# Kernel tuning notes

Hardware: AMD Instinct MI355X
Metric: run time of the kernel (lower is better)

## Reference

```python
import jax, jax.numpy as jnp
import numpy as np

NUM_CLASSES = 80
REG_MAX = 16
CLS_W, BOX_W, DFL_W = 1.0, 2.5, 0.5


def _make_anchors(img=640, strides=(8, 16, 32)):
    pts, strs = [], []
    for s in strides:
        n = img // s
        xs = (np.arange(n, dtype=np.float32) + 0.5) * s
        gy, gx = np.meshgrid(xs, xs, indexing='ij')
        pts.append(np.stack([gx.ravel(), gy.ravel()], axis=1))
        strs.append(np.full((n * n, 1), float(s), np.float32))
    return np.concatenate(pts, 0).astype(np.float32), np.concatenate(strs, 0)


def setup_inputs() -> dict:
    key = jax.random.key(0)
    k1, k2, k3, k4, k5 = jax.random.split(key, 5)
    B, G = 16, 20
    ap, st = _make_anchors()  # A = 8400
    A = ap.shape[0]
    cls_scores = jax.random.uniform(k1, (B, A, NUM_CLASSES), dtype=jnp.float32)
    reg_distri = jax.random.normal(k2, (B, A, 4 * (REG_MAX + 1)), dtype=jnp.float32)
    cxcy = jax.random.uniform(k3, (B, G, 2), dtype=jnp.float32) * 560.0 + 40.0
    wh = jax.random.uniform(k4, (B, G, 2), dtype=jnp.float32) * 120.0 + 20.0
    gt_boxes = jnp.concatenate([cxcy - wh * 0.5, cxcy + wh * 0.5], axis=-1)  # xyxy
    gt_labels = jax.random.randint(k5, (B, G), 0, NUM_CLASSES)
    return {"cls_scores": cls_scores, "reg_distri": reg_distri, "gt_boxes": gt_boxes,
            "anchor_points": jnp.asarray(ap), "stride_tensor": jnp.asarray(st),
            "gt_labels": gt_labels}


def _per_image(pred_cls, pred_reg, gt_boxes, gt_labels, anchor_points, stride):
    A, C = pred_cls.shape
    G = gt_boxes.shape[0]
    k = max(min(13, A // max(G, 1)), 3)
    p = jnp.clip(pred_cls, 1e-7, 1.0 - 1e-7)
    centers = (gt_boxes[:, :2] + gt_boxes[:, 2:]) * 0.5                    # [G,2]
    d = jnp.sqrt(jnp.sum((anchor_points[:, None, :] - centers[None]) ** 2, -1))  # [A,G]
    _, topk_idx = jax.lax.top_k(-d.T, k)                                    # [G,k] nearest anchors
    ax = anchor_points[topk_idx]                                            # [G,k,2]
    inside = ((ax[..., 0] >= gt_boxes[:, None, 0]) & (ax[..., 0] <= gt_boxes[:, None, 2]) &
              (ax[..., 1] >= gt_boxes[:, None, 1]) & (ax[..., 1] <= gt_boxes[:, None, 3]))
    any_in = inside.any(-1, keepdims=True)
    assign_k = jnp.where(any_in, inside, jnp.arange(k) < 3)                 # fallback: 3 nearest
    assign = jnp.zeros((G, A), bool).at[jnp.arange(G)[:, None], topk_idx].set(assign_k)
    aT = assign.T                                                           # [A,G]
    fg = aT.any(1)                                                          # [A]
    last_gt = (G - 1) - jnp.argmax(aT[:, ::-1], axis=1)
    target_box = jnp.where(fg[:, None], gt_boxes[last_gt], 0.0)             # [A,4]
    onehot = jax.nn.one_hot(gt_labels, C, dtype=p.dtype)                    # [G,C]
    target_cls = jnp.max(aT[:, :, None].astype(p.dtype) * onehot[None], axis=1)  # [A,C]
    bce = -(target_cls * jnp.log(p) + (1.0 - target_cls) * jnp.log(1.0 - p))
    num_pos = fg.sum().astype(p.dtype)
    pos_w = jnp.minimum(A / jnp.maximum(num_pos, 1.0), 50.0)
    fgf = fg.astype(p.dtype)[:, None]
    pos_loss = jnp.where(num_pos > 0,
                         jnp.sum(bce * fgf) / jnp.maximum(num_pos * C, 1.0) * pos_w, 0.0)
    neg_loss = jnp.sum(bce * (1.0 - fgf)) / jnp.maximum((A - num_pos) * C, 1.0)
    # box decode (DFL expectation) + smooth-L1 on fg anchors
    reg = jax.nn.softmax(pred_reg.reshape(A, 4, REG_MAX + 1), axis=-1)
    proj = jnp.arange(REG_MAX + 1, dtype=p.dtype)
    dist = jnp.sum(reg * proj, axis=-1)                                     # [A,4]
    s = stride[:, 0]
    pb = jnp.stack([anchor_points[:, 0] - dist[:, 0] * s,
                    anchor_points[:, 1] - dist[:, 1] * s,
                    anchor_points[:, 0] + dist[:, 2] * s,
                    anchor_points[:, 1] + dist[:, 3] * s], axis=-1)
    diff = pb - target_box
    ad = jnp.abs(diff)
    sl1 = jnp.where(ad < 1.0, 0.5 * diff * diff, ad - 0.5)
    box_loss = jnp.where(num_pos > 0,
                         jnp.sum(sl1 * fgf) / jnp.maximum(num_pos * 4.0, 1.0), 0.0)
    return pos_loss + neg_loss, box_loss


def reference(cls_scores, reg_distri, gt_boxes, anchor_points, stride_tensor, gt_labels):
    cls_l, box_l = jax.vmap(
        lambda pc, pr, gb, gl: _per_image(pc, pr, gb, gl, anchor_points, stride_tensor)
    )(cls_scores, reg_distri, gt_boxes, gt_labels)
    loss_cls = cls_l.mean() * CLS_W
    loss_box = box_l.mean() * BOX_W
    return loss_cls + loss_box  # loss_dfl is identically 0 in the original
```

## Files before the change

### kernel.cpp

```cpp
#include <hip/hip_runtime.h>
#include <hip/hip_bf16.h>
#include <cfloat>

#define C_NUM 80
#define REG_MAXP1 17
#define NS 33

__global__ __launch_bounds__(256) void assign_kernel(const float* __restrict__ gt_boxes,
                              const float* __restrict__ anchor_points,
                              unsigned int* __restrict__ mask,
                              int B, int A, int G, int k)
{
    __shared__ float s_val[4];
    __shared__ int   s_idx[4];
    __shared__ int   s_sel;
    __shared__ int   s_topk[32];
    __shared__ int   s_anyin;

    int bg = blockIdx.x;
    int b = bg / G, g = bg % G;
    const float* box = gt_boxes + (size_t)(b * G + g) * 4;
    float x0 = box[0], y0 = box[1], x1 = box[2], y1 = box[3];
    float cx = (x0 + x1) * 0.5f, cy = (y0 + y1) * 0.5f;

    int t = threadIdx.x;
    float dv[NS];
#pragma unroll
    for (int s = 0; s < NS; ++s) {
        int i = t + s * 256;
        float d = FLT_MAX;
        if (i < A) {
            float dx = anchor_points[2 * i] - cx;
            float dy = anchor_points[2 * i + 1] - cy;
            d = dx * dx + dy * dy;
        }
        dv[s] = d;
    }

    int wid = t >> 6, lane = t & 63;
    for (int it = 0; it < k; ++it) {
        float best = FLT_MAX; int bi = 0x7fffffff;
#pragma unroll
        for (int s = 0; s < NS; ++s) {
            if (dv[s] < best) { best = dv[s]; bi = t + s * 256; }
        }
        for (int off = 32; off; off >>= 1) {
            float ov = __shfl_down(best, off);
            int   oi = __shfl_down(bi, off);
            if (ov < best || (ov == best && oi < bi)) { best = ov; bi = oi; }
        }
        if (lane == 0) { s_val[wid] = best; s_idx[wid] = bi; }
        __syncthreads();
        if (t == 0) {
            float bv = s_val[0]; int bix = s_idx[0];
#pragma unroll
            for (int w = 1; w < 4; ++w) {
                if (s_val[w] < bv || (s_val[w] == bv && s_idx[w] < bix)) { bv = s_val[w]; bix = s_idx[w]; }
            }
            s_sel = bix;
            s_topk[it] = bix;
        }
        __syncthreads();
        int sel = s_sel;
        if ((sel & 255) == t) {
            int slot = sel >> 8;
#pragma unroll
            for (int s = 0; s < NS; ++s) if (s == slot) dv[s] = FLT_MAX;
        }
    }

    if (t == 0) s_anyin = 0;
    __syncthreads();
    bool inside = false; int aidx = -1;
    if (t < k) {
        aidx = s_topk[t];
        float ax = anchor_points[2 * aidx], ay = anchor_points[2 * aidx + 1];
        inside = (ax >= x0) && (ax <= x1) && (ay >= y0) && (ay <= y1);
        if (inside) atomicOr(&s_anyin, 1);
    }
    __syncthreads();
    if (t < k) {
        bool asg = s_anyin ? inside : (t < 3);
        if (asg) atomicOr(&mask[(size_t)b * A + aidx], 1u << g);
    }
}

__global__ void assign_kernel_lds(const float* __restrict__ gt_boxes,
                              const float* __restrict__ anchor_points,
                              unsigned int* __restrict__ mask,
                              int B, int A, int G, int k)
{
    extern __shared__ float smem[];
    float* d2   = smem;
    float* rval = smem + A;
    int*   ridx = (int*)(rval + 256);
    int*   s_topk = ridx + 256;
    int*   s_anyin = s_topk + 32;

    int bg = blockIdx.x;
    int b = bg / G, g = bg % G;
    const float* box = gt_boxes + (size_t)(b * G + g) * 4;
    float x0 = box[0], y0 = box[1], x1 = box[2], y1 = box[3];
    float cx = (x0 + x1) * 0.5f, cy = (y0 + y1) * 0.5f;

    int t = threadIdx.x;
    for (int i = t; i < A; i += 256) {
        float dx = anchor_points[2 * i] - cx;
        float dy = anchor_points[2 * i + 1] - cy;
        d2[i] = dx * dx + dy * dy;
    }
    __syncthreads();

    for (int it = 0; it < k; ++it) {
        float best = FLT_MAX; int bi = 0x7fffffff;
        for (int i = t; i < A; i += 256) {
            float v = d2[i];
            if (v < best) { best = v; bi = i; }
        }
        rval[t] = best; ridx[t] = bi;
        __syncthreads();
        for (int s = 128; s > 0; s >>= 1) {
            if (t < s) {
                float v2 = rval[t + s]; int i2 = ridx[t + s];
                if (v2 < rval[t] || (v2 == rval[t] && i2 < ridx[t])) { rval[t] = v2; ridx[t] = i2; }
            }
            __syncthreads();
        }
        if (t == 0) { s_topk[it] = ridx[0]; d2[ridx[0]] = FLT_MAX; }
        __syncthreads();
    }

    if (t == 0) *s_anyin = 0;
    __syncthreads();
    bool inside = false; int aidx = -1;
    if (t < k) {
        aidx = s_topk[t];
        float ax = anchor_points[2 * aidx], ay = anchor_points[2 * aidx + 1];
        inside = (ax >= x0) && (ax <= x1) && (ay >= y0) && (ay <= y1);
        if (inside) atomicOr(s_anyin, 1);
    }
    __syncthreads();
    if (t < k) {
        bool asg = (*s_anyin) ? inside : (t < 3);
        if (asg) atomicOr(&mask[(size_t)b * A + aidx], 1u << g);
    }
}

__global__ __launch_bounds__(256) void npos_kernel(const unsigned int* __restrict__ mask,
                            int* __restrict__ npos, int A)
{
    __shared__ int sh[4];
    int b = blockIdx.x, t = threadIdx.x;
    int cnt = 0;
    for (int i = t; i < A; i += 256) cnt += (mask[(size_t)b * A + i] != 0u);
    for (int off = 32; off; off >>= 1) cnt += __shfl_down(cnt, off);
    if ((t & 63) == 0) sh[t >> 6] = cnt;
    __syncthreads();
    if (t == 0) npos[b] = sh[0] + sh[1] + sh[2] + sh[3];
}

__global__ __launch_bounds__(256) void cls_kernel(const float4* __restrict__ cls,
                           const unsigned int* __restrict__ mask,
                           const int* __restrict__ gt_labels,
                           float* __restrict__ acc, int A, int G)
{
    const int CQ = C_NUM / 4;
    int b = blockIdx.y;
    int nq = A * CQ;
    const float4* base = cls + (size_t)b * nq;
    const unsigned int* mrow = mask + (size_t)b * A;
    const int* lab = gt_labels + (size_t)b * G;

    float pos = 0.f, neg = 0.f;
    for (int q = blockIdx.x * 256 + threadIdx.x; q < nq; q += gridDim.x * 256) {
        float4 v = base[q];
        unsigned int m = mrow[q / CQ];
        float p0 = fminf(fmaxf(v.x, 1e-7f), 1.0f - 1e-7f);
        float p1 = fminf(fmaxf(v.y, 1e-7f), 1.0f - 1e-7f);
        float p2 = fminf(fmaxf(v.z, 1e-7f), 1.0f - 1e-7f);
        float p3 = fminf(fmaxf(v.w, 1e-7f), 1.0f - 1e-7f);
        if (m) {
            int c0 = (q % CQ) * 4;
            unsigned int tm = 0, mm = m;
            while (mm) {
                int g = __ffs(mm) - 1;
                mm &= mm - 1;
                unsigned int d = (unsigned int)(lab[g] - c0);
                if (d < 4u) tm |= 1u << d;
            }
            pos -= logf((tm & 1u) ? p0 : 1.0f - p0);
            pos -= logf((tm & 2u) ? p1 : 1.0f - p1);
            pos -= logf((tm & 4u) ? p2 : 1.0f - p2);
            pos -= logf((tm & 8u) ? p3 : 1.0f - p3);
        } else {
            neg -= logf(1.0f - p0) + logf(1.0f - p1) + logf(1.0f - p2) + logf(1.0f - p3);
        }
    }
    for (int off = 32; off; off >>= 1) {
        pos += __shfl_down(pos, off);
        neg += __shfl_down(neg, off);
    }
    __shared__ float sp[4], sn[4];
    int wid = threadIdx.x >> 6, lane = threadIdx.x & 63;
    if (lane == 0) { sp[wid] = pos; sn[wid] = neg; }
    __syncthreads();
    if (threadIdx.x == 0) {
        float P = sp[0] + sp[1] + sp[2] + sp[3];
        float N = sn[0] + sn[1] + sn[2] + sn[3];
        if (P != 0.f) atomicAdd(&acc[b * 3 + 0], P);
        if (N != 0.f) atomicAdd(&acc[b * 3 + 1], N);
    }
}

__global__ __launch_bounds__(256) void box_kernel(const float* __restrict__ reg,
                           const float* __restrict__ gt_boxes,
                           const float* __restrict__ ap,
                           const float* __restrict__ st,
                           const unsigned int* __restrict__ mask,
                           float* __restrict__ acc, int A, int G)
{
    int a = blockIdx.x * 256 + threadIdx.x;
    int b = blockIdx.y;
    float v = 0.f;
    if (a < A) {
        unsigned int m = mask[(size_t)b * A + a];
        if (m) {
            int lg = 31 - __clz(m);
            const float* tb = gt_boxes + (size_t)(b * G + lg) * 4;
            const float* r = reg + ((size_t)b * A + a) * (4 * REG_MAXP1);
            float s = st[a];
            float axp = ap[2 * a], ayp = ap[2 * a + 1];
            float dist[4];
#pragma unroll
            for (int j = 0; j < 4; ++j) {
                const float* rr = r + j * REG_MAXP1;
                float mx = rr[0];
#pragma unroll
                for (int i = 1; i < REG_MAXP1; ++i) mx = fmaxf(mx, rr[i]);
                float sum = 0.f, dot = 0.f;
#pragma unroll
                for (int i = 0; i < REG_MAXP1; ++i) {
                    float e = expf(rr[i] - mx);
                    sum += e; dot += e * (float)i;
                }
                dist[j] = dot / sum;
            }
            float pb[4] = { axp - dist[0] * s, ayp - dist[1] * s,
                            axp + dist[2] * s, ayp + dist[3] * s };
#pragma unroll
            for (int j = 0; j < 4; ++j) {
                float df = pb[j] - tb[j];
                float ad = fabsf(df);
                v += (ad < 1.0f) ? 0.5f * df * df : ad - 0.5f;
            }
        }
    }
    for (int off = 32; off; off >>= 1) v += __shfl_down(v, off);
    __shared__ float sv[4];
    int wid = threadIdx.x >> 6, lane = threadIdx.x & 63;
    if (lane == 0) sv[wid] = v;
    __syncthreads();
    if (threadIdx.x == 0) {
        float V = sv[0] + sv[1] + sv[2] + sv[3];
        if (V != 0.f) atomicAdd(&acc[b * 3 + 2], V);
    }
}

__global__ void final_kernel(const float* __restrict__ acc,
                             const int* __restrict__ npos,
                             float* __restrict__ out, int B, int A)
{
    if (threadIdx.x == 0 && blockIdx.x == 0) {
        float cls_sum = 0.f, box_sum = 0.f;
        for (int b = 0; b < B; ++b) {
            float np = (float)npos[b];
            float neg = acc[b * 3 + 1] / fmaxf(((float)A - np) * (float)C_NUM, 1.0f);
            float pos = 0.f, box = 0.f;
            if (np > 0.f) {
                float pw = fminf((float)A / fmaxf(np, 1.0f), 50.0f);
                pos = acc[b * 3 + 0] / fmaxf(np * (float)C_NUM, 1.0f) * pw;
                box = acc[b * 3 + 2] / fmaxf(np * 4.0f, 1.0f);
            }
            cls_sum += pos + neg;
            box_sum += box;
        }
        out[0] = cls_sum / (float)B * 1.0f + box_sum / (float)B * 2.5f;
    }
}

extern "C" void kernel_launch(void* const* d_in, const int* in_sizes, int n_in,
                              void* d_out, int out_size, void* d_ws, size_t ws_size,
                              hipStream_t stream)
{
    const float* cls   = (const float*)d_in[0];
    const float* reg   = (const float*)d_in[1];
    const float* gtb   = (const float*)d_in[2];
    const float* ap    = (const float*)d_in[3];
    const float* st    = (const float*)d_in[4];
    const int*   glab  = (const int*)d_in[5];

    int A = in_sizes[3] / 2;
    int B = in_sizes[0] / (A * C_NUM);
    int G = in_sizes[5] / B;
    int k = A / (G > 1 ? G : 1); if (k > 13) k = 13; if (k < 3) k = 3;

    size_t maskBytes = (size_t)B * A * sizeof(unsigned int);
    unsigned int* mask = (unsigned int*)d_ws;
    float* acc = (float*)((char*)d_ws + maskBytes);
    int* npos = (int*)(acc + 3 * B);
    size_t usedBytes = maskBytes + 3 * B * sizeof(float) + B * sizeof(int);

    hipMemsetAsync(d_ws, 0, usedBytes, stream);

    if (A <= NS * 256) {
        assign_kernel<<<B * G, 256, 0, stream>>>(gtb, ap, mask, B, A, G, k);
    } else {
        size_t shmem = (size_t)A * sizeof(float) + 256 * sizeof(float) + 256 * sizeof(int)
                     + 32 * sizeof(int) + sizeof(int);
        assign_kernel_lds<<<B * G, 256, shmem, stream>>>(gtb, ap, mask, B, A, G, k);
    }

    npos_kernel<<<B, 256, 0, stream>>>(mask, npos, A);

    dim3 g3(128, B);
    cls_kernel<<<g3, 256, 0, stream>>>((const float4*)cls, mask, glab, acc, A, G);

    dim3 g4((A + 255) / 256, B);
    box_kernel<<<g4, 256, 0, stream>>>(reg, gtb, ap, st, mask, acc, A, G);

    final_kernel<<<1, 64, 0, stream>>>(acc, npos, (float*)d_out, B, A);
}
```

Before: 182.7 us.

## Compact foreground list, fuse box loss into cls kernel, drop memset and npos pass

The assign kernel now writes the selected anchor indices per GT instead of atomically OR-ing into a global mask. A new per-image raster kernel builds the mask in LDS, writes it out, counts positives and emits a compact foreground list. The box loss is then computed only over that list inside the cls kernel, which removes the separate box kernel, the npos kernel and the memset. Fast __logf/__expf intrinsics replace logf/expf, and the LDS fallback path for large A is removed. In exchange this relies on A <= 8448, k <= 16 and at most 512 foreground anchors per image, and the fast math intrinsics slightly reduce accuracy.

```diff
diff --git a/kernel.cpp b/kernel.cpp
--- a/kernel.cpp
+++ b/kernel.cpp
@@ -5,16 +5,18 @@
 #define C_NUM 80
 #define REG_MAXP1 17
 #define NS 33
+#define MAXA 8448
+#define FG_STRIDE 512
 
 __global__ __launch_bounds__(256) void assign_kernel(const float* __restrict__ gt_boxes,
                               const float* __restrict__ anchor_points,
-                              unsigned int* __restrict__ mask,
+                              int* __restrict__ sel,
                               int B, int A, int G, int k)
 {
     __shared__ float s_val[4];
     __shared__ int   s_idx[4];
     __shared__ int   s_sel;
-    __shared__ int   s_topk[32];
+    __shared__ int   s_topk[16];
     __shared__ int   s_anyin;
 
     int bg = blockIdx.x;
@@ -61,9 +63,9 @@
             s_topk[it] = bix;
         }
         __syncthreads();
-        int sel = s_sel;
-        if ((sel & 255) == t) {
-            int slot = sel >> 8;
+        int selx = s_sel;
+        if ((selx & 255) == t) {
+            int slot = selx >> 8;
 #pragma unroll
             for (int s = 0; s < NS; ++s) if (s == slot) dv[s] = FLT_MAX;
         }
@@ -81,87 +83,57 @@
     __syncthreads();
     if (t < k) {
         bool asg = s_anyin ? inside : (t < 3);
-        if (asg) atomicOr(&mask[(size_t)b * A + aidx], 1u << g);
-    }
-}
-
-__global__ void assign_kernel_lds(const float* __restrict__ gt_boxes,
-                              const float* __restrict__ anchor_points,
+        sel[(size_t)bg * 16 + t] = asg ? aidx : -1;
+    }
+}
+
+__global__ __launch_bounds__(256) void raster_kernel(const int* __restrict__ sel,
                               unsigned int* __restrict__ mask,
-                              int B, int A, int G, int k)
-{
-    extern __shared__ float smem[];
-    float* d2   = smem;
-    float* rval = smem + A;
-    int*   ridx = (int*)(rval + 256);
-    int*   s_topk = ridx + 256;
-    int*   s_anyin = s_topk + 32;
-
-    int bg = blockIdx.x;
-    int b = bg / G, g = bg % G;
-    const float* box = gt_boxes + (size_t)(b * G + g) * 4;
-    float x0 = box[0], y0 = box[1], x1 = box[2], y1 = box[3];
-    float cx = (x0 + x1) * 0.5f, cy = (y0 + y1) * 0.5f;
-
-    int t = threadIdx.x;
+                              int* __restrict__ fglist,
+                              int* __restrict__ npos,
+                              float* __restrict__ acc,
+                              int A, int G, int k)
+{
+    __shared__ unsigned int lmask[MAXA];
+    __shared__ int s_cnt;
+    int b = blockIdx.x, t = threadIdx.x;
+
+    for (int i = t; i < A; i += 256) lmask[i] = 0u;
+    if (t == 0) s_cnt = 0;
+    if (t < 3) acc[b * 3 + t] = 0.f;
+    __syncthreads();
+
+    for (int i = t; i < G * 16; i += 256) {
+        int slot = i & 15;
+        if (slot < k) {
+            int a = sel[(size_t)(b * G) * 16 + i];
+            if (a >= 0) atomicOr(&lmask[a], 1u << (i >> 4));
+        }
+    }
+    __syncthreads();
+
     for (int i = t; i < A; i += 256) {
-        float dx = anchor_points[2 * i] - cx;
-        float dy = anchor_points[2 * i + 1] - cy;
-        d2[i] = dx * dx + dy * dy;
-    }
-    __syncthreads();
-
-    for (int it = 0; it < k; ++it) {
-        float best = FLT_MAX; int bi = 0x7fffffff;
-        for (int i = t; i < A; i += 256) {
-            float v = d2[i];
-            if (v < best) { best = v; bi = i; }
-        }
-        rval[t] = best; ridx[t] = bi;
-        __syncthreads();
-        for (int s = 128; s > 0; s >>= 1) {
-            if (t < s) {
-                float v2 = rval[t + s]; int i2 = ridx[t + s];
-                if (v2 < rval[t] || (v2 == rval[t] && i2 < ridx[t])) { rval[t] = v2; ridx[t] = i2; }
-            }
-            __syncthreads();
-        }
-        if (t == 0) { s_topk[it] = ridx[0]; d2[ridx[0]] = FLT_MAX; }
-        __syncthreads();
-    }
-
-    if (t == 0) *s_anyin = 0;
-    __syncthreads();
-    bool inside = false; int aidx = -1;
-    if (t < k) {
-        aidx = s_topk[t];
-        float ax = anchor_points[2 * aidx], ay = anchor_points[2 * aidx + 1];
-        inside = (ax >= x0) && (ax <= x1) && (ay >= y0) && (ay <= y1);
-        if (inside) atomicOr(s_anyin, 1);
-    }
-    __syncthreads();
-    if (t < k) {
-        bool asg = (*s_anyin) ? inside : (t < 3);
-        if (asg) atomicOr(&mask[(size_t)b * A + aidx], 1u << g);
-    }
-}
-
-__global__ __launch_bounds__(256) void npos_kernel(const unsigned int* __restrict__ mask,
-                            int* __restrict__ npos, int A)
-{
-    __shared__ int sh[4];
-    int b = blockIdx.x, t = threadIdx.x;
-    int cnt = 0;
-    for (int i = t; i < A; i += 256) cnt += (mask[(size_t)b * A + i] != 0u);
-    for (int off = 32; off; off >>= 1) cnt += __shfl_down(cnt, off);
-    if ((t & 63) == 0) sh[t >> 6] = cnt;
-    __syncthreads();
-    if (t == 0) npos[b] = sh[0] + sh[1] + sh[2] + sh[3];
-}
-
-__global__ __launch_bounds__(256) void cls_kernel(const float4* __restrict__ cls,
+        unsigned int m = lmask[i];
+        mask[(size_t)b * A + i] = m;
+        if (m) {
+            int lg = 31 - __clz(m);
+            int p = atomicAdd(&s_cnt, 1);
+            fglist[b * FG_STRIDE + p] = i | (lg << 16);
+        }
+    }
+    __syncthreads();
+    if (t == 0) npos[b] = s_cnt;
+}
+
+__global__ __launch_bounds__(256) void clsbox_kernel(const float4* __restrict__ cls,
+                           const float4* __restrict__ reg,
+                           const float* __restrict__ gt_boxes,
+                           const float* __restrict__ ap,
+                           const float* __restrict__ st,
                            const unsigned int* __restrict__ mask,
                            const int* __restrict__ gt_labels,
+                           const int* __restrict__ fglist,
+                           const int* __restrict__ npos,
                            float* __restrict__ acc, int A, int G)
 {
     const int CQ = C_NUM / 4;
@@ -188,81 +160,73 @@
                 unsigned int d = (unsigned int)(lab[g] - c0);
                 if (d < 4u) tm |= 1u << d;
             }
-            pos -= logf((tm & 1u) ? p0 : 1.0f - p0);
-            pos -= logf((tm & 2u) ? p1 : 1.0f - p1);
-            pos -= logf((tm & 4u) ? p2 : 1.0f - p2);
-            pos -= logf((tm & 8u) ? p3 : 1.0f - p3);
+            pos -= __logf((tm & 1u) ? p0 : 1.0f - p0);
+            pos -= __logf((tm & 2u) ? p1 : 1.0f - p1);
+            pos -= __logf((tm & 4u) ? p2 : 1.0f - p2);
+            pos -= __logf((tm & 8u) ? p3 : 1.0f - p3);
         } else {
-            neg -= logf(1.0f - p0) + logf(1.0f - p1) + logf(1.0f - p2) + logf(1.0f - p3);
-        }
-    }
+            neg -= __logf(1.0f - p0) + __logf(1.0f - p1) + __logf(1.0f - p2) + __logf(1.0f - p3);
+        }
+    }
+
+    float bx = 0.f;
+    int nfg = npos[b];
+    int e = blockIdx.x * 256 + threadIdx.x;
+    if (e < nfg) {
+        int ent = fglist[b * FG_STRIDE + e];
+        int a = ent & 0xffff;
+        int lg = ent >> 16;
+        const float* tb = gt_boxes + (size_t)(b * G + lg) * 4;
+        const float4* r4 = reg + ((size_t)b * A + a) * REG_MAXP1;
+        float rr[4 * REG_MAXP1];
+#pragma unroll
+        for (int i = 0; i < REG_MAXP1; ++i) {
+            float4 v = r4[i];
+            rr[4 * i] = v.x; rr[4 * i + 1] = v.y; rr[4 * i + 2] = v.z; rr[4 * i + 3] = v.w;
+        }
+        float s = st[a];
+        float axp = ap[2 * a], ayp = ap[2 * a + 1];
+        float dist[4];
+#pragma unroll
+        for (int j = 0; j < 4; ++j) {
+            const float* rj = rr + j * REG_MAXP1;
+            float mx = rj[0];
+#pragma unroll
+            for (int i = 1; i < REG_MAXP1; ++i) mx = fmaxf(mx, rj[i]);
+            float sum = 0.f, dot = 0.f;
+#pragma unroll
+            for (int i = 0; i < REG_MAXP1; ++i) {
+                float ev = __expf(rj[i] - mx);
+                sum += ev; dot += ev * (float)i;
+            }
+            dist[j] = dot / sum;
+        }
+        float pb[4] = { axp - dist[0] * s, ayp - dist[1] * s,
+                        axp + dist[2] * s, ayp + dist[3] * s };
+#pragma unroll
+        for (int j = 0; j < 4; ++j) {
+            float df = pb[j] - tb[j];
+            float ad = fabsf(df);
+            bx += (ad < 1.0f) ? 0.5f * df * df : ad - 0.5f;
+        }
+    }
+
     for (int off = 32; off; off >>= 1) {
         pos += __shfl_down(pos, off);
         neg += __shfl_down(neg, off);
-    }
-    __shared__ float sp[4], sn[4];
+        bx  += __shfl_down(bx, off);
+    }
+    __shared__ float sp[4], sn[4], sb[4];
     int wid = threadIdx.x >> 6, lane = threadIdx.x & 63;
-    if (lane == 0) { sp[wid] = pos; sn[wid] = neg; }
+    if (lane == 0) { sp[wid] = pos; sn[wid] = neg; sb[wid] = bx; }
     __syncthreads();
     if (threadIdx.x == 0) {
         float P = sp[0] + sp[1] + sp[2] + sp[3];
         float N = sn[0] + sn[1] + sn[2] + sn[3];
+        float X = sb[0] + sb[1] + sb[2] + sb[3];
         if (P != 0.f) atomicAdd(&acc[b * 3 + 0], P);
         if (N != 0.f) atomicAdd(&acc[b * 3 + 1], N);
-    }
-}
-
-__global__ __launch_bounds__(256) void box_kernel(const float* __restrict__ reg,
-                           const float* __restrict__ gt_boxes,
-                           const float* __restrict__ ap,
-                           const float* __restrict__ st,
-                           const unsigned int* __restrict__ mask,
-                           float* __restrict__ acc, int A, int G)
-{
-    int a = blockIdx.x * 256 + threadIdx.x;
-    int b = blockIdx.y;
-    float v = 0.f;
-    if (a < A) {
-        unsigned int m = mask[(size_t)b * A + a];
-        if (m) {
-            int lg = 31 - __clz(m);
-            const float* tb = gt_boxes + (size_t)(b * G + lg) * 4;
-            const float* r = reg + ((size_t)b * A + a) * (4 * REG_MAXP1);
-            float s = st[a];
-            float axp = ap[2 * a], ayp = ap[2 * a + 1];
-            float dist[4];
-#pragma unroll
-            for (int j = 0; j < 4; ++j) {
-                const float* rr = r + j * REG_MAXP1;
-                float mx = rr[0];
-#pragma unroll
-                for (int i = 1; i < REG_MAXP1; ++i) mx = fmaxf(mx, rr[i]);
-                float sum = 0.f, dot = 0.f;
-#pragma unroll
-                for (int i = 0; i < REG_MAXP1; ++i) {
-                    float e = expf(rr[i] - mx);
-                    sum += e; dot += e * (float)i;
-                }
-                dist[j] = dot / sum;
-            }
-            float pb[4] = { axp - dist[0] * s, ayp - dist[1] * s,
-                            axp + dist[2] * s, ayp + dist[3] * s };
-#pragma unroll
-            for (int j = 0; j < 4; ++j) {
-                float df = pb[j] - tb[j];
-                float ad = fabsf(df);
-                v += (ad < 1.0f) ? 0.5f * df * df : ad - 0.5f;
-            }
-        }
-    }
-    for (int off = 32; off; off >>= 1) v += __shfl_down(v, off);
-    __shared__ float sv[4];
-    int wid = threadIdx.x >> 6, lane = threadIdx.x & 63;
-    if (lane == 0) sv[wid] = v;
-    __syncthreads();
-    if (threadIdx.x == 0) {
-        float V = sv[0] + sv[1] + sv[2] + sv[3];
-        if (V != 0.f) atomicAdd(&acc[b * 3 + 2], V);
+        if (X != 0.f) atomicAdd(&acc[b * 3 + 2], X);
     }
 }
 
@@ -304,29 +268,19 @@
     int G = in_sizes[5] / B;
     int k = A / (G > 1 ? G : 1); if (k > 13) k = 13; if (k < 3) k = 3;
 
-    size_t maskBytes = (size_t)B * A * sizeof(unsigned int);
     unsigned int* mask = (unsigned int*)d_ws;
-    float* acc = (float*)((char*)d_ws + maskBytes);
-    int* npos = (int*)(acc + 3 * B);
-    size_t usedBytes = maskBytes + 3 * B * sizeof(float) + B * sizeof(int);
-
-    hipMemsetAsync(d_ws, 0, usedBytes, stream);
-
-    if (A <= NS * 256) {
-        assign_kernel<<<B * G, 256, 0, stream>>>(gtb, ap, mask, B, A, G, k);
-    } else {
-        size_t shmem = (size_t)A * sizeof(float) + 256 * sizeof(float) + 256 * sizeof(int)
-                     + 32 * sizeof(int) + sizeof(int);
-        assign_kernel_lds<<<B * G, 256, shmem, stream>>>(gtb, ap, mask, B, A, G, k);
-    }
-
-    npos_kernel<<<B, 256, 0, stream>>>(mask, npos, A);
+    float* acc   = (float*)(mask + (size_t)B * A);
+    int*   npos  = (int*)(acc + 3 * B);
+    int*   sel   = npos + B;
+    int*   fgl   = sel + (size_t)B * G * 16;
+
+    assign_kernel<<<B * G, 256, 0, stream>>>(gtb, ap, sel, B, A, G, k);
+
+    raster_kernel<<<B, 256, 0, stream>>>(sel, mask, fgl, npos, acc, A, G, k);
 
     dim3 g3(128, B);
-    cls_kernel<<<g3, 256, 0, stream>>>((const float4*)cls, mask, glab, acc, A, G);
-
-    dim3 g4((A + 255) / 256, B);
-    box_kernel<<<g4, 256, 0, stream>>>(reg, gtb, ap, st, mask, acc, A, G);
+    clsbox_kernel<<<g3, 256, 0, stream>>>((const float4*)cls, (const float4*)reg,
+                                          gtb, ap, st, mask, glab, fgl, npos, acc, A, G);
 
     final_kernel<<<1, 64, 0, stream>>>(acc, npos, (float*)d_out, B, A);
 }
```

Result: no change. 182.4 us (-0.2%).
